# Kernel optimization log

Measured on AMD Instinct MI355X. Metric: run time of the kernel, lower is better.

The kernel has to match this reference:

```python
import jax, jax.numpy as jnp
import numpy as np

BATCH_SIZE_PER_IM = 512
FG_FRACTION = 0.25
FG_THRESH = 0.5
BG_THRESH_HI = 0.5
BG_THRESH_LO = 0.0
MAX_FG = int(FG_FRACTION * BATCH_SIZE_PER_IM)  # 128


def _rand_boxes(key, shape):
    a = jax.random.uniform(key, shape + (4,), dtype=jnp.float32)
    ymin = jnp.minimum(a[..., 0], a[..., 2])
    ymax = jnp.maximum(a[..., 0], a[..., 2]) + 1e-3
    xmin = jnp.minimum(a[..., 1], a[..., 3])
    xmax = jnp.maximum(a[..., 1], a[..., 3]) + 1e-3
    return jnp.stack([ymin, xmin, ymax, xmax], axis=-1)


def setup_inputs() -> dict:
    key = jax.random.key(0)
    k1, k2, k3, k4 = jax.random.split(key, 4)
    B, N, G = 32, 8192, 128
    boxes = _rand_boxes(k1, (B, N))
    gt_boxes = _rand_boxes(k2, (B, G))
    gt_labels = jax.random.randint(k3, (B, G), 0, 91, dtype=jnp.int32)
    noise = jax.random.uniform(k4, (B, N + G), dtype=jnp.float32)
    return {"boxes": boxes, "gt_boxes": gt_boxes, "gt_labels": gt_labels, "noise": noise}


def _bbox_overlap(boxes, gt_boxes):
    # boxes: [B, M, 4], gt_boxes: [B, G, 4], layout (ymin, xmin, ymax, xmax)
    b_ymin, b_xmin, b_ymax, b_xmax = [boxes[..., i:i + 1] for i in range(4)]  # [B,M,1]
    g_ymin, g_xmin, g_ymax, g_xmax = [gt_boxes[..., i][:, None, :] for i in range(4)]  # [B,1,G]
    i_ymin = jnp.maximum(b_ymin, g_ymin)
    i_xmin = jnp.maximum(b_xmin, g_xmin)
    i_ymax = jnp.minimum(b_ymax, g_ymax)
    i_xmax = jnp.minimum(b_xmax, g_xmax)
    i_area = jnp.maximum(i_ymax - i_ymin, 0.0) * jnp.maximum(i_xmax - i_xmin, 0.0)  # [B,M,G]
    b_area = (b_ymax - b_ymin) * (b_xmax - b_xmin)           # [B,M,1]
    g_area = (g_ymax - g_ymin) * (g_xmax - g_xmin)           # [B,1,G]
    iou = i_area / (b_area + g_area - i_area)
    # padded gt boxes (filled with -1) get IoU = -1
    padding = jnp.logical_and(i_ymin < 0, i_xmin < 0)
    return jnp.where(padding, -1.0, iou)


def reference(boxes, gt_boxes, gt_labels, noise):
    boxes = jax.lax.stop_gradient(boxes)
    all_boxes = jnp.concatenate([boxes, gt_boxes], axis=1)        # [B, M=N+G, 4]
    iou = _bbox_overlap(all_boxes, gt_boxes)                      # [B, M, G]
    max_ov = jnp.max(iou, axis=2)                                 # [B, M]
    p2l = jnp.argmax(iou, axis=2).astype(jnp.int32)               # [B, M]
    box_t = jnp.take_along_axis(gt_boxes, p2l[..., None], axis=1)  # [B, M, 4]
    cls_t = jnp.take_along_axis(gt_labels, p2l, axis=1)           # [B, M]
    pos = max_ov > FG_THRESH
    neg = jnp.logical_and(max_ov >= BG_THRESH_LO, max_ov < BG_THRESH_HI)
    cls_t = jnp.where(neg, 0, cls_t)
    box_t = jnp.where(neg[..., None], 0.0, box_t)
    p2l = jnp.where(neg, 0, p2l)
    # --- balanced fg/bg subsampling (random scores provided in `noise`) ---
    pos_score = jnp.where(pos, noise, -1.0)
    kth = jax.lax.top_k(pos_score, MAX_FG)[0][:, -1:]             # [B,1] threshold
    sel_pos = jnp.logical_and(pos, pos_score >= kth)              # at most MAX_FG fg
    # selected fg get priority band 2+, bg band [0,1), rest -1
    combined = jnp.where(sel_pos, 2.0 + noise, jnp.where(neg, noise, -1.0))
    _, idx = jax.lax.top_k(combined, BATCH_SIZE_PER_IM)           # [B, K]
    rois = jnp.take_along_axis(all_boxes, idx[..., None], axis=1)      # [B, K, 4]
    sample_box_t = jnp.take_along_axis(box_t, idx[..., None], axis=1)  # [B, K, 4]
    sample_cls_t = jnp.take_along_axis(cls_t, idx, axis=1)             # [B, K]
    sample_p2l = jnp.take_along_axis(p2l, idx, axis=1)                 # [B, K]
    return sample_box_t, sample_cls_t, rois, sample_p2l
```

## Files before the change

kernel.cpp:

```cpp
#include <hip/hip_runtime.h>
#include <stdint.h>

#define BATCH 32
#define NBOX 8192
#define NGT 128
#define M (NBOX + NGT)
#define K_OUT 512
#define MAX_FG 128
#define C_CAP 256
#define S_CAP 256
#define U_CAP 1024

__device__ __forceinline__ unsigned int bkt1024(float ns) {
    unsigned int u = (unsigned int)(ns * 16777216.0f) >> 14;
    return u > 1023u ? 1023u : u;
}

template <typename F>
__device__ __forceinline__ void wave_compact(bool pred, unsigned int* ctr,
                                             unsigned int cap, F writer) {
    unsigned long long mb = __ballot(pred);
    if (!mb) return;
    const int lane = threadIdx.x & 63;
    const int leader = __ffsll((unsigned long long)mb) - 1;
    unsigned int base = 0;
    if (lane == leader) base = atomicAdd(ctr, (unsigned int)__popcll(mb));
    base = __shfl(base, leader, 64);
    if (pred) {
        unsigned int slot = base + (unsigned int)__popcll(mb & ((1ull << lane) - 1ull));
        if (slot < cap) writer(slot);
    }
}

__global__ __launch_bounds__(128) void iou_kernel(
    const float* __restrict__ boxes,
    const float* __restrict__ gt_boxes,
    unsigned short* __restrict__ packed)
{
    const int b = blockIdx.x / 65;
    const int m = (blockIdx.x % 65) * 128 + threadIdx.x;

    const float4* __restrict__ gt4 = (const float4*)gt_boxes + b * NGT;

    float4 bb = (m < NBOX) ? ((const float4*)boxes)[b * NBOX + m]
                           : gt4[m - NBOX];
    float b_area = __fmul_rn(__fsub_rn(bb.z, bb.x), __fsub_rn(bb.w, bb.y));

    float best = -1e30f;
    int bidx = 0;
    #pragma unroll 8
    for (int g = 0; g < NGT; ++g) {
        float4 gg = gt4[g];
        float ga = __fmul_rn(__fsub_rn(gg.z, gg.x), __fsub_rn(gg.w, gg.y));
        float iymin = fmaxf(bb.x, gg.x);
        float ixmin = fmaxf(bb.y, gg.y);
        float iymax = fminf(bb.z, gg.z);
        float ixmax = fminf(bb.w, gg.w);
        float ia  = __fmul_rn(fmaxf(__fsub_rn(iymax, iymin), 0.0f),
                              fmaxf(__fsub_rn(ixmax, ixmin), 0.0f));
        float den = __fsub_rn(__fadd_rn(b_area, ga), ia);
        float iou = __fdiv_rn(ia, den);
        if (iou > best) { best = iou; bidx = g; }
    }
    bool pos = best > 0.5f;
    bool neg = (best >= 0.0f) && (best < 0.5f);
    packed[b * M + m] = (unsigned short)(bidx | (neg ? 256 : 0) | (pos ? 512 : 0));
}

__global__ __launch_bounds__(1024) void select_kernel(
    const float* __restrict__ boxes,
    const float* __restrict__ gt_boxes,
    const int*   __restrict__ gt_labels,
    const float* __restrict__ noise,
    const unsigned short* __restrict__ packed,
    float* __restrict__ out)
{
    const int b = blockIdx.x;
    const int tid = threadIdx.x;

    __shared__ float sh_ns[M];
    __shared__ unsigned int hist[1024];
    __shared__ unsigned int hist2[1024];
    __shared__ unsigned char posmask[M / 8];
    __shared__ unsigned char negmask[M / 8];
    __shared__ float4 sgt[NGT];
    __shared__ int slab[NGT];
    __shared__ float C[C_CAP];
    __shared__ unsigned short slist[S_CAP];
    __shared__ __align__(16) unsigned int   ukey[U_CAP + 4];
    __shared__ __align__(16) unsigned short um[U_CAP + 4];
    __shared__ unsigned int sh_Bp, sh_needp, sh_cc, sh_n1a, sh_B, sh_cnt, sh_kth;

    float* out_bt  = out;
    float* out_cls = out + BATCH * K_OUT * 4;
    float* out_roi = out + BATCH * K_OUT * 5;
    float* out_p2l = out + BATCH * K_OUT * 9;

    hist[tid] = 0;
    hist2[tid] = 0;
    if (tid == 0) { sh_cc = 0; sh_n1a = 0; sh_B = 0; sh_cnt = 0; sh_kth = 0xBF800000u; }
    if (tid < NGT) {
        sgt[tid]  = ((const float4*)gt_boxes)[b * NGT + tid];
        slab[tid] = gt_labels[b * NGT + tid];
    }
    __syncthreads();

    float f[8];
    unsigned int pb = 0, nb = 0;
    {
        const uint4*  pk4 = (const uint4*)(packed + (size_t)b * M);
        const float4* ns4 = (const float4*)(noise + (size_t)b * M);
        {
            uint4 pv = pk4[tid];
            float4 n0 = ns4[2 * tid], n1v = ns4[2 * tid + 1];
            ((float4*)sh_ns)[2 * tid] = n0;
            ((float4*)sh_ns)[2 * tid + 1] = n1v;
            f[0] = n0.x; f[1] = n0.y; f[2] = n0.z; f[3] = n0.w;
            f[4] = n1v.x; f[5] = n1v.y; f[6] = n1v.z; f[7] = n1v.w;
            unsigned short e[8];
            e[0] = (unsigned short)(pv.x & 0xFFFF); e[1] = (unsigned short)(pv.x >> 16);
            e[2] = (unsigned short)(pv.y & 0xFFFF); e[3] = (unsigned short)(pv.y >> 16);
            e[4] = (unsigned short)(pv.z & 0xFFFF); e[5] = (unsigned short)(pv.z >> 16);
            e[6] = (unsigned short)(pv.w & 0xFFFF); e[7] = (unsigned short)(pv.w >> 16);
            #pragma unroll
            for (int k = 0; k < 8; ++k) {
                if (e[k] & 512) {
                    pb |= (1u << k);
                    atomicAdd(&hist2[bkt1024(f[k])], 1u);
                } else if (e[k] & 256) {
                    nb |= (1u << k);
                    atomicAdd(&hist[bkt1024(f[k])], 1u);
                }
            }
            posmask[tid] = (unsigned char)pb;
            negmask[tid] = (unsigned char)nb;
        }
        if (tid < 16) {
            int c = 1024 + tid;
            uint4 pv = pk4[c];
            float4 n0 = ns4[2 * c], n1v = ns4[2 * c + 1];
            ((float4*)sh_ns)[2 * c] = n0;
            ((float4*)sh_ns)[2 * c + 1] = n1v;
            float ft[8] = {n0.x, n0.y, n0.z, n0.w, n1v.x, n1v.y, n1v.z, n1v.w};
            unsigned short e[8];
            e[0] = (unsigned short)(pv.x & 0xFFFF); e[1] = (unsigned short)(pv.x >> 16);
            e[2] = (unsigned short)(pv.y & 0xFFFF); e[3] = (unsigned short)(pv.y >> 16);
            e[4] = (unsigned short)(pv.z & 0xFFFF); e[5] = (unsigned short)(pv.z >> 16);
            e[6] = (unsigned short)(pv.w & 0xFFFF); e[7] = (unsigned short)(pv.w >> 16);
            unsigned int pb2 = 0, nb2 = 0;
            #pragma unroll
            for (int k = 0; k < 8; ++k) {
                if (e[k] & 512) {
                    pb2 |= (1u << k);
                    atomicAdd(&hist2[bkt1024(ft[k])], 1u);
                } else if (e[k] & 256) {
                    nb2 |= (1u << k);
                    atomicAdd(&hist[bkt1024(ft[k])], 1u);
                }
            }
            posmask[c] = (unsigned char)pb2;
            negmask[c] = (unsigned char)nb2;
        }
    }
    __syncthreads();

    {
        const int wv = tid >> 6, ln = tid & 63;
        if (wv < 2) {
            unsigned int* H = wv ? hist2 : hist;
            unsigned int s[16];
            #pragma unroll
            for (int k = 0; k < 16; ++k) {
                unsigned int v = H[k * 64 + ln];
                #pragma unroll
                for (int off = 1; off < 64; off <<= 1) {
                    unsigned int o = __shfl_down(v, off, 64);
                    if (ln + off < 64) v += o;
                }
                s[k] = v;
            }
            unsigned int after = 0;
            #pragma unroll
            for (int k = 15; k >= 0; --k) {
                unsigned int tot = __shfl(s[k], 0, 64);
                H[k * 64 + ln] = s[k] + after;
                after += tot;
            }
        }
    }
    __syncthreads();
    const unsigned int nneg = hist[0];
    const unsigned int npos = hist2[0];

    if (npos >= MAX_FG) {
        {
            unsigned int S  = hist2[tid];
            unsigned int Sn = (tid < 1023) ? hist2[tid + 1] : 0;
            if (S >= MAX_FG && Sn < MAX_FG) { sh_Bp = tid; sh_needp = MAX_FG - Sn; }
        }
        __syncthreads();
        const unsigned int Bp = sh_Bp, needp = sh_needp;
        #pragma unroll
        for (int k = 0; k < 8; ++k) {
            if (((pb >> k) & 1u) && bkt1024(f[k]) == Bp) {
                unsigned int slot = atomicAdd(&sh_cc, 1u);
                if (slot < C_CAP) C[slot] = f[k];
            }
        }
        if (tid < 16) {
            unsigned int pb2 = posmask[1024 + tid];
            #pragma unroll
            for (int k = 0; k < 8; ++k) {
                if ((pb2 >> k) & 1u) {
                    float v = sh_ns[(1024 + tid) * 8 + k];
                    if (bkt1024(v) == Bp) {
                        unsigned int slot = atomicAdd(&sh_cc, 1u);
                        if (slot < C_CAP) C[slot] = v;
                    }
                }
            }
        }
        __syncthreads();
        {
            unsigned int cc = min(sh_cc, (unsigned int)C_CAP);
            if (tid < (int)cc) {
                float my = C[tid];
                unsigned int g = 0, e = 0;
                for (unsigned int j = 0; j < cc; ++j) {
                    float v = C[j];
                    g += (v > my) ? 1u : 0u;
                    e += (v == my) ? 1u : 0u;
                }
                if (g < needp && g + e >= needp) sh_kth = __float_as_uint(my);
            }
        }
        __syncthreads();
    }
    const float kthf = __uint_as_float(sh_kth);

    #pragma unroll
    for (int k = 0; k < 8; ++k) {
        if (((pb >> k) & 1u) && f[k] >= kthf) {
            unsigned int slot = atomicAdd(&sh_n1a, 1u);
            if (slot < S_CAP) slist[slot] = (unsigned short)(tid * 8 + k);
        }
    }
    if (tid < 16) {
        unsigned int pb2 = posmask[1024 + tid];
        #pragma unroll
        for (int k = 0; k < 8; ++k) {
            if ((pb2 >> k) & 1u) {
                int m = (1024 + tid) * 8 + k;
                if (sh_ns[m] >= kthf) {
                    unsigned int slot = atomicAdd(&sh_n1a, 1u);
                    if (slot < S_CAP) slist[slot] = (unsigned short)m;
                }
            }
        }
    }
    __syncthreads();
    const unsigned int n1 = min(sh_n1a, (unsigned int)S_CAP);
    const unsigned int k2 = K_OUT - n1;
    const bool enough_neg = (nneg >= k2);

    if (enough_neg) {
        unsigned int S  = hist[tid];
        unsigned int Sn = (tid < 1023) ? hist[tid + 1] : 0;
        if (S >= k2 && Sn < k2) sh_B = tid;
    }
    if (tid < (int)n1) {
        int mi = slist[tid];
        float nsi = sh_ns[mi];
        float ci = __fadd_rn(2.0f, nsi);
        unsigned int r = 0;
        for (unsigned int j = 0; j < n1; ++j) {
            int mj = slist[j];
            float cj = __fadd_rn(2.0f, sh_ns[mj]);
            if (cj > ci || (cj == ci && mj < mi)) ++r;
        }
        int pkv = packed[(size_t)b * M + mi];
        int lbl = pkv & 127;
        float4 roi = (mi < NBOX) ? ((const float4*)boxes)[b * NBOX + mi]
                                 : sgt[mi - NBOX];
        ((float4*)out_bt)[b * K_OUT + r] = sgt[lbl];
        out_cls[b * K_OUT + r] = (float)slab[lbl];
        ((float4*)out_roi)[b * K_OUT + r] = roi;
        out_p2l[b * K_OUT + r] = (float)lbl;
    }
    __syncthreads();
    const unsigned int B1 = sh_B;

    #pragma unroll
    for (int k = 0; k < 8; ++k) {
        float v = f[k];
        bool p = ((nb >> k) & 1u) && bkt1024(v) >= B1;
        unsigned short mm = (unsigned short)(tid * 8 + k);
        wave_compact(p, &sh_cnt, U_CAP, [&](unsigned int s) {
            ukey[s] = __float_as_uint(v);
            um[s]   = mm;
        });
    }
    {
        unsigned int nb2 = (tid < 16) ? (unsigned int)negmask[1024 + tid] : 0u;
        #pragma unroll
        for (int k = 0; k < 8; ++k) {
            bool p = (nb2 >> k) & 1u;
            float v = p ? sh_ns[(1024 + tid) * 8 + k] : 0.0f;
            p = p && bkt1024(v) >= B1;
            unsigned short mm = (unsigned short)((1024 + tid) * 8 + k);
            wave_compact(p, &sh_cnt, U_CAP, [&](unsigned int s) {
                ukey[s] = __float_as_uint(v);
                um[s]   = mm;
            });
        }
    }
    __syncthreads();

    const unsigned int q = min(sh_cnt, (unsigned int)U_CAP);
    if (tid < 4) { ukey[q + tid] = 0u; um[q + tid] = 0xFFFFu; }
    __syncthreads();
    for (unsigned int i = tid; i < q; i += 1024) {
        unsigned int ki = ukey[i];
        unsigned short mi = um[i];
        unsigned int r = 0;
        for (unsigned int j = 0; j < q; j += 4) {
            uint4 kv = *(const uint4*)&ukey[j];
            ushort4 mv = *(const ushort4*)&um[j];
            r += (kv.x > ki || (kv.x == ki && mv.x < mi)) ? 1u : 0u;
            r += (kv.y > ki || (kv.y == ki && mv.y < mi)) ? 1u : 0u;
            r += (kv.z > ki || (kv.z == ki && mv.z < mi)) ? 1u : 0u;
            r += (kv.w > ki || (kv.w == ki && mv.w < mi)) ? 1u : 0u;
        }
        if (r < k2) {
            float4 roi = (mi < NBOX) ? ((const float4*)boxes)[b * NBOX + mi]
                                     : sgt[mi - NBOX];
            unsigned int gr = n1 + r;
            ((float4*)out_bt)[b * K_OUT + gr] = make_float4(0.f, 0.f, 0.f, 0.f);
            out_cls[b * K_OUT + gr] = 0.0f;
            ((float4*)out_roi)[b * K_OUT + gr] = roi;
            out_p2l[b * K_OUT + gr] = 0.0f;
        }
    }

    if (!enough_neg) {
        __syncthreads();
        const unsigned int k3 = k2 - nneg;
        for (int m = tid; m < M; m += 1024) {
            if (((posmask[m >> 3] >> (m & 7)) & 1) && sh_ns[m] < kthf) {
                unsigned int r = 0;
                for (int m2 = 0; m2 < m; ++m2)
                    if (((posmask[m2 >> 3] >> (m2 & 7)) & 1) && sh_ns[m2] < kthf) ++r;
                if (r < k3) {
                    int pkv = packed[(size_t)b * M + m];
                    int lbl = pkv & 127;
                    float4 roi = (m < NBOX) ? ((const float4*)boxes)[b * NBOX + m]
                                            : sgt[m - NBOX];
                    unsigned int gr = n1 + nneg + r;
                    ((float4*)out_bt)[b * K_OUT + gr] = sgt[lbl];
                    out_cls[b * K_OUT + gr] = (float)slab[lbl];
                    ((float4*)out_roi)[b * K_OUT + gr] = roi;
                    out_p2l[b * K_OUT + gr] = (float)lbl;
                }
            }
        }
    }
}

extern "C" void kernel_launch(void* const* d_in, const int* in_sizes, int n_in,
                              void* d_out, int out_size, void* d_ws, size_t ws_size,
                              hipStream_t stream) {
    const float* boxes     = (const float*)d_in[0];
    const float* gt_boxes  = (const float*)d_in[1];
    const int*   gt_labels = (const int*)d_in[2];
    const float* noise     = (const float*)d_in[3];
    unsigned short* packed = (unsigned short*)d_ws;
    float* out = (float*)d_out;

    iou_kernel<<<BATCH * 65, 128, 0, stream>>>(boxes, gt_boxes, packed);
    select_kernel<<<BATCH, 1024, 0, stream>>>(boxes, gt_boxes, gt_labels, noise,
                                              packed, out);
}
```

Baseline: 121.1 us.

## Stage GT boxes in LDS, two proposals per thread, bucket-scatter negative ranking

The IoU kernel now loads the GT boxes and their areas into shared memory once per block and has each thread handle two proposals, so the GT data and area math are reused. In the select kernel, negative candidates are scattered into bucket-ordered slots using the suffix-sum histogram. Each candidate is then ranked only against entries in its own bucket, replacing the full O(q^2) comparison. The positive ranking stores precomputed keys and uses vectorized comparisons. This adds more shared memory and atomics per bucket, and depends on the hist array holding suffix counts.

```diff
diff --git a/kernel.cpp b/kernel.cpp
--- a/kernel.cpp
+++ b/kernel.cpp
@@ -11,60 +11,84 @@
 #define S_CAP 256
 #define U_CAP 1024
 
+#define IOU_TPB 256
+#define IOU_VPT 2
+#define IOU_SPAN (IOU_TPB * IOU_VPT)
+#define IOU_BPB ((M + IOU_SPAN - 1) / IOU_SPAN)
+
 __device__ __forceinline__ unsigned int bkt1024(float ns) {
     unsigned int u = (unsigned int)(ns * 16777216.0f) >> 14;
     return u > 1023u ? 1023u : u;
 }
 
-template <typename F>
-__device__ __forceinline__ void wave_compact(bool pred, unsigned int* ctr,
-                                             unsigned int cap, F writer) {
-    unsigned long long mb = __ballot(pred);
-    if (!mb) return;
-    const int lane = threadIdx.x & 63;
-    const int leader = __ffsll((unsigned long long)mb) - 1;
-    unsigned int base = 0;
-    if (lane == leader) base = atomicAdd(ctr, (unsigned int)__popcll(mb));
-    base = __shfl(base, leader, 64);
-    if (pred) {
-        unsigned int slot = base + (unsigned int)__popcll(mb & ((1ull << lane) - 1ull));
-        if (slot < cap) writer(slot);
-    }
-}
-
-__global__ __launch_bounds__(128) void iou_kernel(
+__global__ __launch_bounds__(256) void iou_kernel(
     const float* __restrict__ boxes,
     const float* __restrict__ gt_boxes,
     unsigned short* __restrict__ packed)
 {
-    const int b = blockIdx.x / 65;
-    const int m = (blockIdx.x % 65) * 128 + threadIdx.x;
-
-    const float4* __restrict__ gt4 = (const float4*)gt_boxes + b * NGT;
-
-    float4 bb = (m < NBOX) ? ((const float4*)boxes)[b * NBOX + m]
-                           : gt4[m - NBOX];
-    float b_area = __fmul_rn(__fsub_rn(bb.z, bb.x), __fsub_rn(bb.w, bb.y));
-
-    float best = -1e30f;
-    int bidx = 0;
-    #pragma unroll 8
+    const int b   = blockIdx.x / IOU_BPB;
+    const int blk = blockIdx.x % IOU_BPB;
+    const int t   = threadIdx.x;
+
+    __shared__ float4 sgt[NGT];
+    __shared__ float  sga[NGT];
+    if (t < NGT) {
+        float4 g = ((const float4*)gt_boxes)[b * NGT + t];
+        sgt[t] = g;
+        sga[t] = __fmul_rn(__fsub_rn(g.z, g.x), __fsub_rn(g.w, g.y));
+    }
+    __syncthreads();
+
+    const int m0 = blk * IOU_SPAN + t;
+    const int m1 = m0 + IOU_TPB;
+    const bool v0 = m0 < M, v1 = m1 < M;
+
+    float4 bb0 = make_float4(0.f, 0.f, 1.f, 1.f);
+    float4 bb1 = make_float4(0.f, 0.f, 1.f, 1.f);
+    if (v0) bb0 = (m0 < NBOX) ? ((const float4*)boxes)[b * NBOX + m0] : sgt[m0 - NBOX];
+    if (v1) bb1 = (m1 < NBOX) ? ((const float4*)boxes)[b * NBOX + m1] : sgt[m1 - NBOX];
+    float a0 = __fmul_rn(__fsub_rn(bb0.z, bb0.x), __fsub_rn(bb0.w, bb0.y));
+    float a1 = __fmul_rn(__fsub_rn(bb1.z, bb1.x), __fsub_rn(bb1.w, bb1.y));
+
+    float best0 = -1e30f, best1 = -1e30f;
+    int i0 = 0, i1 = 0;
+    #pragma unroll 4
     for (int g = 0; g < NGT; ++g) {
-        float4 gg = gt4[g];
-        float ga = __fmul_rn(__fsub_rn(gg.z, gg.x), __fsub_rn(gg.w, gg.y));
-        float iymin = fmaxf(bb.x, gg.x);
-        float ixmin = fmaxf(bb.y, gg.y);
-        float iymax = fminf(bb.z, gg.z);
-        float ixmax = fminf(bb.w, gg.w);
-        float ia  = __fmul_rn(fmaxf(__fsub_rn(iymax, iymin), 0.0f),
-                              fmaxf(__fsub_rn(ixmax, ixmin), 0.0f));
-        float den = __fsub_rn(__fadd_rn(b_area, ga), ia);
-        float iou = __fdiv_rn(ia, den);
-        if (iou > best) { best = iou; bidx = g; }
-    }
-    bool pos = best > 0.5f;
-    bool neg = (best >= 0.0f) && (best < 0.5f);
-    packed[b * M + m] = (unsigned short)(bidx | (neg ? 256 : 0) | (pos ? 512 : 0));
+        float4 gg = sgt[g];
+        float  ga = sga[g];
+        {
+            float iymin = fmaxf(bb0.x, gg.x);
+            float ixmin = fmaxf(bb0.y, gg.y);
+            float iymax = fminf(bb0.z, gg.z);
+            float ixmax = fminf(bb0.w, gg.w);
+            float ia  = __fmul_rn(fmaxf(__fsub_rn(iymax, iymin), 0.0f),
+                                  fmaxf(__fsub_rn(ixmax, ixmin), 0.0f));
+            float den = __fsub_rn(__fadd_rn(a0, ga), ia);
+            float iou = __fdiv_rn(ia, den);
+            if (iou > best0) { best0 = iou; i0 = g; }
+        }
+        {
+            float iymin = fmaxf(bb1.x, gg.x);
+            float ixmin = fmaxf(bb1.y, gg.y);
+            float iymax = fminf(bb1.z, gg.z);
+            float ixmax = fminf(bb1.w, gg.w);
+            float ia  = __fmul_rn(fmaxf(__fsub_rn(iymax, iymin), 0.0f),
+                                  fmaxf(__fsub_rn(ixmax, ixmin), 0.0f));
+            float den = __fsub_rn(__fadd_rn(a1, ga), ia);
+            float iou = __fdiv_rn(ia, den);
+            if (iou > best1) { best1 = iou; i1 = g; }
+        }
+    }
+    if (v0) {
+        bool pos = best0 > 0.5f;
+        bool neg = (best0 >= 0.0f) && (best0 < 0.5f);
+        packed[b * M + m0] = (unsigned short)(i0 | (neg ? 256 : 0) | (pos ? 512 : 0));
+    }
+    if (v1) {
+        bool pos = best1 > 0.5f;
+        bool neg = (best1 >= 0.0f) && (best1 < 0.5f);
+        packed[b * M + m1] = (unsigned short)(i1 | (neg ? 256 : 0) | (pos ? 512 : 0));
+    }
 }
 
 __global__ __launch_bounds__(1024) void select_kernel(
@@ -81,15 +105,17 @@
     __shared__ float sh_ns[M];
     __shared__ unsigned int hist[1024];
     __shared__ unsigned int hist2[1024];
+    __shared__ unsigned int bctr[1024];
     __shared__ unsigned char posmask[M / 8];
     __shared__ unsigned char negmask[M / 8];
     __shared__ float4 sgt[NGT];
     __shared__ int slab[NGT];
     __shared__ float C[C_CAP];
-    __shared__ unsigned short slist[S_CAP];
-    __shared__ __align__(16) unsigned int   ukey[U_CAP + 4];
-    __shared__ __align__(16) unsigned short um[U_CAP + 4];
-    __shared__ unsigned int sh_Bp, sh_needp, sh_cc, sh_n1a, sh_B, sh_cnt, sh_kth;
+    __shared__ __align__(16) unsigned int   skey[S_CAP + 4];
+    __shared__ __align__(16) unsigned short sm[S_CAP + 4];
+    __shared__ unsigned int   ukey[U_CAP];
+    __shared__ unsigned short um[U_CAP];
+    __shared__ unsigned int sh_Bp, sh_needp, sh_cc, sh_n1a, sh_B, sh_kth;
 
     float* out_bt  = out;
     float* out_cls = out + BATCH * K_OUT * 4;
@@ -98,7 +124,8 @@
 
     hist[tid] = 0;
     hist2[tid] = 0;
-    if (tid == 0) { sh_cc = 0; sh_n1a = 0; sh_B = 0; sh_cnt = 0; sh_kth = 0xBF800000u; }
+    bctr[tid] = 0;
+    if (tid == 0) { sh_cc = 0; sh_n1a = 0; sh_B = 0; sh_kth = 0xBF800000u; }
     if (tid < NGT) {
         sgt[tid]  = ((const float4*)gt_boxes)[b * NGT + tid];
         slab[tid] = gt_labels[b * NGT + tid];
@@ -242,7 +269,10 @@
     for (int k = 0; k < 8; ++k) {
         if (((pb >> k) & 1u) && f[k] >= kthf) {
             unsigned int slot = atomicAdd(&sh_n1a, 1u);
-            if (slot < S_CAP) slist[slot] = (unsigned short)(tid * 8 + k);
+            if (slot < S_CAP) {
+                skey[slot] = __float_as_uint(__fadd_rn(2.0f, f[k]));
+                sm[slot]   = (unsigned short)(tid * 8 + k);
+            }
         }
     }
     if (tid < 16) {
@@ -251,9 +281,13 @@
         for (int k = 0; k < 8; ++k) {
             if ((pb2 >> k) & 1u) {
                 int m = (1024 + tid) * 8 + k;
-                if (sh_ns[m] >= kthf) {
+                float v = sh_ns[m];
+                if (v >= kthf) {
                     unsigned int slot = atomicAdd(&sh_n1a, 1u);
-                    if (slot < S_CAP) slist[slot] = (unsigned short)m;
+                    if (slot < S_CAP) {
+                        skey[slot] = __float_as_uint(__fadd_rn(2.0f, v));
+                        sm[slot]   = (unsigned short)m;
+                    }
                 }
             }
         }
@@ -263,73 +297,85 @@
     const unsigned int k2 = K_OUT - n1;
     const bool enough_neg = (nneg >= k2);
 
+    if (tid < 4) { skey[n1 + tid] = 0u; sm[n1 + tid] = 0xFFFFu; }
     if (enough_neg) {
         unsigned int S  = hist[tid];
         unsigned int Sn = (tid < 1023) ? hist[tid + 1] : 0;
         if (S >= k2 && Sn < k2) sh_B = tid;
     }
+    __syncthreads();
+    const unsigned int B1 = sh_B;
+
     if (tid < (int)n1) {
-        int mi = slist[tid];
-        float nsi = sh_ns[mi];
-        float ci = __fadd_rn(2.0f, nsi);
+        unsigned int   ki = skey[tid];
+        unsigned short mi = sm[tid];
         unsigned int r = 0;
-        for (unsigned int j = 0; j < n1; ++j) {
-            int mj = slist[j];
-            float cj = __fadd_rn(2.0f, sh_ns[mj]);
-            if (cj > ci || (cj == ci && mj < mi)) ++r;
-        }
-        int pkv = packed[(size_t)b * M + mi];
+        for (unsigned int j = 0; j < n1; j += 4) {
+            uint4   kv = *(const uint4*)&skey[j];
+            ushort4 mv = *(const ushort4*)&sm[j];
+            r += (kv.x > ki || (kv.x == ki && mv.x < mi)) ? 1u : 0u;
+            r += (kv.y > ki || (kv.y == ki && mv.y < mi)) ? 1u : 0u;
+            r += (kv.z > ki || (kv.z == ki && mv.z < mi)) ? 1u : 0u;
+            r += (kv.w > ki || (kv.w == ki && mv.w < mi)) ? 1u : 0u;
+        }
+        int mi_ = mi;
+        int pkv = packed[(size_t)b * M + mi_];
         int lbl = pkv & 127;
-        float4 roi = (mi < NBOX) ? ((const float4*)boxes)[b * NBOX + mi]
-                                 : sgt[mi - NBOX];
+        float4 roi = (mi_ < NBOX) ? ((const float4*)boxes)[b * NBOX + mi_]
+                                  : sgt[mi_ - NBOX];
         ((float4*)out_bt)[b * K_OUT + r] = sgt[lbl];
         out_cls[b * K_OUT + r] = (float)slab[lbl];
         ((float4*)out_roi)[b * K_OUT + r] = roi;
         out_p2l[b * K_OUT + r] = (float)lbl;
     }
-    __syncthreads();
-    const unsigned int B1 = sh_B;
 
     #pragma unroll
     for (int k = 0; k < 8; ++k) {
-        float v = f[k];
-        bool p = ((nb >> k) & 1u) && bkt1024(v) >= B1;
-        unsigned short mm = (unsigned short)(tid * 8 + k);
-        wave_compact(p, &sh_cnt, U_CAP, [&](unsigned int s) {
-            ukey[s] = __float_as_uint(v);
-            um[s]   = mm;
-        });
-    }
-    {
-        unsigned int nb2 = (tid < 16) ? (unsigned int)negmask[1024 + tid] : 0u;
+        if ((nb >> k) & 1u) {
+            float v = f[k];
+            unsigned int be = bkt1024(v);
+            if (be >= B1) {
+                unsigned int base = (be < 1023) ? hist[be + 1] : 0;
+                unsigned int a = base + atomicAdd(&bctr[be], 1u);
+                if (a < U_CAP) {
+                    ukey[a] = __float_as_uint(v);
+                    um[a]   = (unsigned short)(tid * 8 + k);
+                }
+            }
+        }
+    }
+    if (tid < 16) {
+        unsigned int nb2 = negmask[1024 + tid];
         #pragma unroll
         for (int k = 0; k < 8; ++k) {
-            bool p = (nb2 >> k) & 1u;
-            float v = p ? sh_ns[(1024 + tid) * 8 + k] : 0.0f;
-            p = p && bkt1024(v) >= B1;
-            unsigned short mm = (unsigned short)((1024 + tid) * 8 + k);
-            wave_compact(p, &sh_cnt, U_CAP, [&](unsigned int s) {
-                ukey[s] = __float_as_uint(v);
-                um[s]   = mm;
-            });
-        }
-    }
-    __syncthreads();
-
-    const unsigned int q = min(sh_cnt, (unsigned int)U_CAP);
-    if (tid < 4) { ukey[q + tid] = 0u; um[q + tid] = 0xFFFFu; }
-    __syncthreads();
-    for (unsigned int i = tid; i < q; i += 1024) {
-        unsigned int ki = ukey[i];
-        unsigned short mi = um[i];
-        unsigned int r = 0;
-        for (unsigned int j = 0; j < q; j += 4) {
-            uint4 kv = *(const uint4*)&ukey[j];
-            ushort4 mv = *(const ushort4*)&um[j];
-            r += (kv.x > ki || (kv.x == ki && mv.x < mi)) ? 1u : 0u;
-            r += (kv.y > ki || (kv.y == ki && mv.y < mi)) ? 1u : 0u;
-            r += (kv.z > ki || (kv.z == ki && mv.z < mi)) ? 1u : 0u;
-            r += (kv.w > ki || (kv.w == ki && mv.w < mi)) ? 1u : 0u;
+            if ((nb2 >> k) & 1u) {
+                int m = (1024 + tid) * 8 + k;
+                float v = sh_ns[m];
+                unsigned int be = bkt1024(v);
+                if (be >= B1) {
+                    unsigned int base = (be < 1023) ? hist[be + 1] : 0;
+                    unsigned int a = base + atomicAdd(&bctr[be], 1u);
+                    if (a < U_CAP) {
+                        ukey[a] = __float_as_uint(v);
+                        um[a]   = (unsigned short)m;
+                    }
+                }
+            }
+        }
+    }
+    __syncthreads();
+
+    const unsigned int q = min(hist[B1], (unsigned int)U_CAP);
+    for (unsigned int a = tid; a < q; a += 1024) {
+        unsigned int   ki = ukey[a];
+        unsigned short mi = um[a];
+        unsigned int be = bkt1024(__uint_as_float(ki));
+        unsigned int base = (be < 1023) ? hist[be + 1] : 0;
+        unsigned int end  = min(hist[be], q);
+        unsigned int r = base;
+        for (unsigned int j = base; j < end; ++j) {
+            unsigned int kj = ukey[j];
+            if (kj > ki || (kj == ki && um[j] < mi)) ++r;
         }
         if (r < k2) {
             float4 roi = (mi < NBOX) ? ((const float4*)boxes)[b * NBOX + mi]
@@ -376,7 +422,7 @@
     unsigned short* packed = (unsigned short*)d_ws;
     float* out = (float*)d_out;
 
-    iou_kernel<<<BATCH * 65, 128, 0, stream>>>(boxes, gt_boxes, packed);
+    iou_kernel<<<BATCH * IOU_BPB, IOU_TPB, 0, stream>>>(boxes, gt_boxes, packed);
     select_kernel<<<BATCH, 1024, 0, stream>>>(boxes, gt_boxes, gt_labels, noise,
                                               packed, out);
 }
```

Measured after the change: 115.9 us. -4.3%, faster.
